# Performance work log

Measured on AMD Instinct MI355X. Metric: run time of the kernel, lower is better.

The kernel has to match this reference:

```python
import jax, jax.numpy as jnp
import numpy as np
import math

B, T, P, E, H = 4, 64, 256, 512, 8
D = E // H
LN_EPS = 1e-5


def setup_inputs() -> dict:
    key = jax.random.key(0)
    ks = jax.random.split(key, 6)
    s = 0.02  # weight init scale
    return {
        "x": jax.random.normal(ks[0], (B, T, P, E), jnp.float32),
        "Wq": jax.random.normal(ks[1], (E, E), jnp.float32) * s,
        "bq": jnp.zeros((E,), jnp.float32),
        "Wk": jax.random.normal(ks[2], (E, E), jnp.float32) * s,
        "bk": jnp.zeros((E,), jnp.float32),
        "Wv": jax.random.normal(ks[3], (E, E), jnp.float32) * s,
        "bv": jnp.zeros((E,), jnp.float32),
        "Wo": jax.random.normal(ks[4], (E, E), jnp.float32) * s,
        "bo": jnp.zeros((E,), jnp.float32),
        "ln_g": jnp.ones((E,), jnp.float32),
        "ln_b": jnp.zeros((E,), jnp.float32),
    }


def _proj(x, W, b):
    # torch nn.Linear: y = x @ W.T + b
    return jnp.einsum('btpe,fe->btpf', x, W) + b


def _heads(y):
    # b t p (h d) -> b p h t d
    b, t, p, e = y.shape
    return y.reshape(b, t, p, H, D).transpose(0, 2, 3, 1, 4)


def reference(x, Wq, bq, Wk, bk, Wv, bv, Wo, bo, ln_g, ln_b):
    b, t, p, e = x.shape
    q = _heads(_proj(x, Wq, bq))  # [B,P,H,T,D]
    k = _heads(_proj(x, Wk, bk))
    v = _heads(_proj(x, Wv, bv))

    scores = jnp.einsum('bphtd,bphsd->bphts', q, k) / math.sqrt(D)
    causal_mask = jnp.triu(jnp.ones((t, t), dtype=bool), k=1)  # True above diag
    scores = jnp.where(causal_mask, -jnp.inf, scores)
    attn = jax.nn.softmax(scores, axis=-1)
    o = jnp.einsum('bphts,bphsd->bphtd', attn, v)

    # b p h t d -> b t p (h d)
    o = o.transpose(0, 3, 1, 2, 4).reshape(b, t, p, e)
    attn_out = jnp.einsum('btpe,fe->btpf', o, Wo) + bo

    y = x + attn_out
    # AdaptiveNormalizer with conditioning=None -> plain LayerNorm over E
    mu = jnp.mean(y, axis=-1, keepdims=True)
    var = jnp.var(y, axis=-1, keepdims=True)
    return (y - mu) * jax.lax.rsqrt(var + LN_EPS) * ln_g + ln_b
```

## Files before the change

### kernel.cpp

```cpp
#include <hip/hip_runtime.h>
#include <stdint.h>

#define B_ 4
#define T_ 64
#define P_ 256
#define E_ 512
#define H_ 8
#define D_ 64
#define NF 1536
#define MCH 16384

typedef unsigned short u16;
typedef __attribute__((ext_vector_type(8))) __bf16 bf16x8;
typedef __attribute__((ext_vector_type(4))) float f32x4;

__device__ __forceinline__ u16 f2bf(float x) {
  union { float f; uint32_t u; } a; a.f = x;
  uint32_t u = a.u;
  uint32_t r = (u + 0x7FFFu + ((u >> 16) & 1u)) >> 16;
  return (u16)r;
}

__device__ __forceinline__ bf16x8 ld8(const u16* p) {
  union { uint4 u; bf16x8 b; } t;
  t.u = *reinterpret_cast<const uint4*>(p);
  return t.b;
}

typedef __attribute__((address_space(3))) void lds_void;
typedef __attribute__((address_space(1))) void g_void;
__device__ __forceinline__ void gl_lds16(const void* g, void* l) {
  __builtin_amdgcn_global_load_lds((g_void*)g, (lds_void*)l, 16, 0, 0);
}

__device__ __forceinline__ f32x4 mfma16(bf16x8 a, bf16x8 b, f32x4 c) {
  return __builtin_amdgcn_mfma_f32_16x16x32_bf16(a, b, c, 0, 0, 0);
}

#define SBAR() __builtin_amdgcn_s_barrier()

__global__ void cvt_bf16(const float* __restrict__ src, u16* __restrict__ dst, int n8) {
  int i = blockIdx.x * blockDim.x + threadIdx.x;
  if (i >= n8) return;
  const float4* s = reinterpret_cast<const float4*>(src) + (size_t)i * 2;
  float4 a = s[0], b = s[1];
  union { u16 u[8]; uint4 v; } t;
  t.u[0] = f2bf(a.x); t.u[1] = f2bf(a.y); t.u[2] = f2bf(a.z); t.u[3] = f2bf(a.w);
  t.u[4] = f2bf(b.x); t.u[5] = f2bf(b.y); t.u[6] = f2bf(b.z); t.u[7] = f2bf(b.w);
  reinterpret_cast<uint4*>(dst)[i] = t.v;
}

__global__ void cvt_w(const float* __restrict__ Wq, const float* __restrict__ Wk,
                      const float* __restrict__ Wv, const float* __restrict__ Wo,
                      u16* __restrict__ wqkv, u16* __restrict__ wobf) {
  int idx = blockIdx.x * blockDim.x + threadIdx.x;
  int w = idx >> 15;
  int off = idx & 32767;
  const float* s = (w == 0) ? Wq : (w == 1) ? Wk : (w == 2) ? Wv : Wo;
  const float4* sp = reinterpret_cast<const float4*>(s) + (size_t)off * 2;
  float4 a = sp[0], b = sp[1];
  union { u16 u[8]; uint4 v; } t;
  t.u[0] = f2bf(a.x); t.u[1] = f2bf(a.y); t.u[2] = f2bf(a.z); t.u[3] = f2bf(a.w);
  t.u[4] = f2bf(b.x); t.u[5] = f2bf(b.y); t.u[6] = f2bf(b.z); t.u[7] = f2bf(b.w);
  if (w < 3) reinterpret_cast<uint4*>(wqkv)[w * 32768 + off] = t.v;
  else       reinterpret_cast<uint4*>(wobf)[off] = t.v;
}

#define K1_MFMA(MB)                                                         \
  __builtin_amdgcn_s_setprio(1);                                            \
  _Pragma("unroll") for (int i = 0; i < 4; i++)                             \
  _Pragma("unroll") for (int j = 0; j < 4; j++)                             \
    acc[(MB) + i][j] = mfma16(af[i], bfv[j], acc[(MB) + i][j]);             \
  __builtin_amdgcn_s_setprio(0);

#define K1_READA(E, HH, MB)                                                 \
  _Pragma("unroll") for (int i = 0; i < 4; i++)                             \
    af[i] = ld8(ldsA + ((E) * 2 + (HH)) * 8192 +                            \
                (wr * 128 + ((MB) + i) * 16 + l15) * 32 + xr8);

#define K1_READB(E, HH)                                                     \
  _Pragma("unroll") for (int j = 0; j < 4; j++)                             \
    bfv[j] = ld8(ldsB + ((E) * 2 + (HH)) * 8192 +                           \
                 (wc * 64 + j * 16 + l15) * 32 + xr8);

__global__ __launch_bounds__(512, 2) void k1_qkv(
    const u16* __restrict__ xbf,
    const u16* __restrict__ wqkv,
    const float* __restrict__ bq, const float* __restrict__ bk, const float* __restrict__ bv,
    u16* __restrict__ qkv)
{
  __shared__ u16 lds[65536];
  u16* ldsA = lds;
  u16* ldsB = lds + 32768;

  const int tid = threadIdx.x;
  const int lane = tid & 63, wid = tid >> 6;
  const int wr = wid >> 2, wc = wid & 3;
  const int g4 = lane >> 4, l15 = lane & 15;
  const int xr8 = (g4 ^ ((l15 >> 1) & 3)) * 8;

  const int cpx = gridDim.x >> 3;
  const int logical = (blockIdx.x & 7) * cpx + (blockIdx.x >> 3);
  const int m0 = (logical / 6) * 256;
  const int n0 = (logical % 6) * 256;

  const u16* ga = xbf + (size_t)m0 * E_;
  const u16* gb = wqkv + (size_t)n0 * E_;

  const int r0 = tid >> 2;
  const int c0 = ((tid & 3) ^ ((tid >> 3) & 3)) * 8;

  auto stageA = [&](int e, int h, int kt) {
    const int kc = kt * 64 + h * 32;
    u16* base = ldsA + (e * 2 + h) * 8192;
    gl_lds16(ga + (size_t)r0 * E_ + kc + c0, base + wid * 512);
    gl_lds16(ga + (size_t)(r0 + 128) * E_ + kc + c0, base + 4096 + wid * 512);
  };
  auto stageB = [&](int e, int h, int kt) {
    const int kc = kt * 64 + h * 32;
    u16* base = ldsB + (e * 2 + h) * 8192;
    gl_lds16(gb + (size_t)r0 * E_ + kc + c0, base + wid * 512);
    gl_lds16(gb + (size_t)(r0 + 128) * E_ + kc + c0, base + 4096 + wid * 512);
  };

  f32x4 acc[8][4];
#pragma unroll
  for (int i = 0; i < 8; i++)
#pragma unroll
    for (int j = 0; j < 4; j++) { f32x4 z = {0.f, 0.f, 0.f, 0.f}; acc[i][j] = z; }

  stageA(0, 0, 0); stageB(0, 0, 0);
  stageA(0, 1, 0); stageB(0, 1, 0);
  stageA(1, 0, 1); stageB(1, 0, 1);
  asm volatile("s_waitcnt vmcnt(8)" ::: "memory");
  SBAR();

#pragma unroll 2
  for (int s = 0; s < 8; ++s) {
    const int e = s & 1;
    bf16x8 af[4], bfv[4];
    K1_READA(e, 0, 0)
    K1_READB(e, 0)
    if (s < 7) stageA(e ^ 1, 1, s + 1);
    SBAR();
    K1_MFMA(0)
    SBAR();
    K1_READA(e, 0, 4)
    if (s < 7) stageB(e ^ 1, 1, s + 1);
    if (s < 7) { asm volatile("s_waitcnt vmcnt(8)" ::: "memory"); }
    else       { asm volatile("s_waitcnt vmcnt(0)" ::: "memory"); }
    SBAR();
    K1_MFMA(4)
    SBAR();
    K1_READA(e, 1, 0)
    K1_READB(e, 1)
    if (s < 6) stageA(e, 0, s + 2);
    SBAR();
    K1_MFMA(0)
    SBAR();
    K1_READA(e, 1, 4)
    if (s < 6) stageB(e, 0, s + 2);
    if (s < 6)      { asm volatile("s_waitcnt vmcnt(8)" ::: "memory"); }
    else if (s == 6){ asm volatile("s_waitcnt vmcnt(4)" ::: "memory"); }
    SBAR();
    K1_MFMA(4)
    SBAR();
  }

  float bias4[4];
#pragma unroll
  for (int ni = 0; ni < 4; ni++) {
    const int fcol = n0 + wc * 64 + ni * 16 + l15;
    bias4[ni] = fcol < 512 ? bq[fcol] : (fcol < 1024 ? bk[fcol - 512] : bv[fcol - 1024]);
  }
  const int fbase = n0 + wc * 64 + l15;
#pragma unroll
  for (int mi = 0; mi < 8; mi++)
#pragma unroll
    for (int r = 0; r < 4; r++) {
      const size_t row = m0 + wr * 128 + mi * 16 + g4 * 4 + r;
      u16* dst = qkv + row * NF + fbase;
#pragma unroll
      for (int ni = 0; ni < 4; ni++)
        dst[ni * 16] = f2bf(acc[mi][ni][r] + bias4[ni]);
    }
}

__global__ __launch_bounds__(256) void k2_attn(
    const u16* __restrict__ qkv,
    u16* __restrict__ o)
{
  __shared__ u16 Pl[4][64 * 72];
  const int tid = threadIdx.x, lane = tid & 63, wid = tid >> 6;
  const int gw = blockIdx.x * 4 + wid;
  const int b = gw >> 11;
  const int g = gw & 2047;
  const int h = g & 7, p = g >> 3;
  const int g4 = lane >> 4;
  const size_t ts = (size_t)P_ * NF;
  const u16* qb = qkv + (size_t)b * MCH * NF + (size_t)p * NF + h * D_;
  const u16* kb = qb + 512;
  const u16* vb = qb + 1024;
  u16* ob = o + (size_t)b * MCH * E_;

  bf16x8 qf[4][2], kf[4][2];
#pragma unroll
  for (int i = 0; i < 4; i++)
#pragma unroll
    for (int ks = 0; ks < 2; ks++) {
      const int rr = i * 16 + (lane & 15);
      const int dc = ks * 32 + g4 * 8;
      qf[i][ks] = ld8(qb + (size_t)rr * ts + dc);
      kf[i][ks] = ld8(kb + (size_t)rr * ts + dc);
    }
  f32x4 S[4][4];
#pragma unroll
  for (int i = 0; i < 4; i++)
#pragma unroll
    for (int j = 0; j < 4; j++) { f32x4 z = {0.f, 0.f, 0.f, 0.f}; S[i][j] = z; }
#pragma unroll
  for (int ks = 0; ks < 2; ks++)
#pragma unroll
    for (int mi = 0; mi < 4; mi++)
#pragma unroll
      for (int ni = 0; ni < 4; ni++)
        S[mi][ni] = mfma16(qf[mi][ks], kf[ni][ks], S[mi][ni]);

  u16* pw = &Pl[wid][0];
#pragma unroll
  for (int mi = 0; mi < 4; mi++)
#pragma unroll
    for (int r = 0; r < 4; r++) {
      const int t = mi * 16 + g4 * 4 + r;
      float v[4]; float mx = -1e30f;
#pragma unroll
      for (int ni = 0; ni < 4; ni++) {
        const int s = ni * 16 + (lane & 15);
        v[ni] = (s <= t) ? S[mi][ni][r] * 0.125f : -1e30f;
        mx = fmaxf(mx, v[ni]);
      }
      mx = fmaxf(mx, __shfl_xor(mx, 1));
      mx = fmaxf(mx, __shfl_xor(mx, 2));
      mx = fmaxf(mx, __shfl_xor(mx, 4));
      mx = fmaxf(mx, __shfl_xor(mx, 8));
      float sum = 0.f; float pv[4];
#pragma unroll
      for (int ni = 0; ni < 4; ni++) {
        const int s = ni * 16 + (lane & 15);
        pv[ni] = (s <= t) ? __expf(v[ni] - mx) : 0.f;
        sum += pv[ni];
      }
      sum += __shfl_xor(sum, 1);
      sum += __shfl_xor(sum, 2);
      sum += __shfl_xor(sum, 4);
      sum += __shfl_xor(sum, 8);
      const float inv = 1.0f / sum;
#pragma unroll
      for (int ni = 0; ni < 4; ni++) {
        const int s = ni * 16 + (lane & 15);
        pw[t * 72 + s] = f2bf(pv[ni] * inv);
      }
    }
  __syncthreads();

  f32x4 O[4][4];
#pragma unroll
  for (int i = 0; i < 4; i++)
#pragma unroll
    for (int j = 0; j < 4; j++) { f32x4 z = {0.f, 0.f, 0.f, 0.f}; O[i][j] = z; }
#pragma unroll
  for (int ks = 0; ks < 2; ks++) {
    bf16x8 pa[4], vf[4];
#pragma unroll
    for (int mi = 0; mi < 4; mi++)
      pa[mi] = ld8(pw + (mi * 16 + (lane & 15)) * 72 + ks * 32 + g4 * 8);
#pragma unroll
    for (int ni = 0; ni < 4; ni++) {
      union { u16 u[8]; bf16x8 b; } tv;
#pragma unroll
      for (int j = 0; j < 8; j++) {
        const int s = ks * 32 + g4 * 8 + j;
        tv.u[j] = vb[(size_t)s * ts + ni * 16 + (lane & 15)];
      }
      vf[ni] = tv.b;
    }
#pragma unroll
    for (int mi = 0; mi < 4; mi++)
#pragma unroll
      for (int ni = 0; ni < 4; ni++)
        O[mi][ni] = mfma16(pa[mi], vf[ni], O[mi][ni]);
  }
#pragma unroll
  for (int mi = 0; mi < 4; mi++)
#pragma unroll
    for (int ni = 0; ni < 4; ni++)
#pragma unroll
      for (int r = 0; r < 4; r++) {
        const int t = mi * 16 + g4 * 4 + r;
        const int d = ni * 16 + (lane & 15);
        ob[((size_t)t * P_ + p) * E_ + h * D_ + d] = f2bf(O[mi][ni][r]);
      }
}

__global__ __launch_bounds__(512) void k3_out(
    const u16* __restrict__ obf,
    const u16* __restrict__ wo,
    const float* __restrict__ bo,
    const float* __restrict__ x,
    const float* __restrict__ lng, const float* __restrict__ lnb,
    float* __restrict__ out)
{
  __shared__ u16 As[2][128 * 32];
  __shared__ u16 Bs[2][512 * 32];
  __shared__ float redS[128][8];
  __shared__ float redQ[128][8];
  const int tid = threadIdx.x, lane = tid & 63, wid = tid >> 6;
  const int m0 = blockIdx.x * 128;
  const int g4 = lane >> 4, l15 = lane & 15;
  const int lr = lane >> 2;
  const int lc = (lane & 3) * 8;

  f32x4 acc[8][4];
#pragma unroll
  for (int i = 0; i < 8; i++)
#pragma unroll
    for (int j = 0; j < 4; j++) { f32x4 z = {0.f, 0.f, 0.f, 0.f}; acc[i][j] = z; }

  const u16* ga = obf + (size_t)m0 * E_;

  auto stage = [&](int buf, int kt) {
    const int k0 = kt * 32;
    gl_lds16(ga + (size_t)(wid * 16 + lr) * E_ + k0 + lc, &As[buf][wid * 512]);
#pragma unroll
    for (int p = 0; p < 4; ++p) {
      const int ch = wid * 4 + p;
      gl_lds16(wo + (size_t)(ch * 16 + lr) * E_ + k0 + lc, &Bs[buf][ch * 512]);
    }
  };

  stage(0, 0);
  __syncthreads();
  int cur = 0;
  for (int kt = 0; kt < 16; ++kt) {
    if (kt < 15) stage(cur ^ 1, kt + 1);
    const int fc = g4 * 8;
    bf16x8 af[8], bfr[4];
#pragma unroll
    for (int mi = 0; mi < 8; mi++) af[mi] = ld8(&As[cur][(mi * 16 + l15) * 32 + fc]);
#pragma unroll
    for (int ni = 0; ni < 4; ni++) bfr[ni] = ld8(&Bs[cur][(wid * 64 + ni * 16 + l15) * 32 + fc]);
#pragma unroll
    for (int mi = 0; mi < 8; mi++)
#pragma unroll
      for (int ni = 0; ni < 4; ni++)
        acc[mi][ni] = mfma16(af[mi], bfr[ni], acc[mi][ni]);
    __syncthreads();
    cur ^= 1;
  }

  float gg[4], bb[4], bof[4];
#pragma unroll
  for (int ni = 0; ni < 4; ni++) {
    const int f = wid * 64 + ni * 16 + l15;
    gg[ni] = lng[f]; bb[ni] = lnb[f]; bof[ni] = bo[f];
  }
#pragma unroll
  for (int mi = 0; mi < 8; mi++)
#pragma unroll
    for (int r = 0; r < 4; r++) {
      const int n = m0 + mi * 16 + g4 * 4 + r;
#pragma unroll
      for (int ni = 0; ni < 4; ni++) {
        const int f = wid * 64 + ni * 16 + l15;
        acc[mi][ni][r] += bof[ni] + x[(size_t)n * E_ + f];
      }
    }
#pragma unroll
  for (int mi = 0; mi < 8; mi++)
#pragma unroll
    for (int r = 0; r < 4; r++) {
      float s = 0.f, q = 0.f;
#pragma unroll
      for (int ni = 0; ni < 4; ni++) { const float y = acc[mi][ni][r]; s += y; q += y * y; }
      s += __shfl_xor(s, 1); q += __shfl_xor(q, 1);
      s += __shfl_xor(s, 2); q += __shfl_xor(q, 2);
      s += __shfl_xor(s, 4); q += __shfl_xor(q, 4);
      s += __shfl_xor(s, 8); q += __shfl_xor(q, 8);
      if (l15 == 0) {
        const int rl = mi * 16 + g4 * 4 + r;
        redS[rl][wid] = s; redQ[rl][wid] = q;
      }
    }
  __syncthreads();
#pragma unroll
  for (int mi = 0; mi < 8; mi++)
#pragma unroll
    for (int r = 0; r < 4; r++) {
      const int rl = mi * 16 + g4 * 4 + r;
      float Sx = 0.f, Qx = 0.f;
#pragma unroll
      for (int w = 0; w < 8; w++) { Sx += redS[rl][w]; Qx += redQ[rl][w]; }
      const float mean = Sx * (1.0f / 512.0f);
      const float var = Qx * (1.0f / 512.0f) - mean * mean;
      const float rs = rsqrtf(var + 1e-5f);
      const int n = m0 + rl;
#pragma unroll
      for (int ni = 0; ni < 4; ni++) {
        const int f = wid * 64 + ni * 16 + l15;
        out[(size_t)n * E_ + f] = (acc[mi][ni][r] - mean) * rs * gg[ni] + bb[ni];
      }
    }
}

extern "C" void kernel_launch(void* const* d_in, const int* in_sizes, int n_in,
                              void* d_out, int out_size, void* d_ws, size_t ws_size,
                              hipStream_t stream) {
  const float* x   = (const float*)d_in[0];
  const float* Wq  = (const float*)d_in[1];
  const float* bq  = (const float*)d_in[2];
  const float* Wk  = (const float*)d_in[3];
  const float* bk  = (const float*)d_in[4];
  const float* Wv  = (const float*)d_in[5];
  const float* bv  = (const float*)d_in[6];
  const float* Wo  = (const float*)d_in[7];
  const float* bo  = (const float*)d_in[8];
  const float* lng = (const float*)d_in[9];
  const float* lnb = (const float*)d_in[10];
  float* out = (float*)d_out;
  uint8_t* ws = (uint8_t*)d_ws;

  const size_t NEED_BIG = 270532608ULL;
  if (ws_size >= NEED_BIG) {
    u16* wqkv = (u16*)(ws);
    u16* wobf = (u16*)(ws + 1572864);
    u16* xbf  = (u16*)(ws + 2097152);
    u16* qkvc = (u16*)(ws + 69206016);
    u16* obf  = xbf;

    cvt_w<<<512, 256, 0, stream>>>(Wq, Wk, Wv, Wo, wqkv, wobf);
    cvt_bf16<<<16384, 256, 0, stream>>>(x, xbf, B_ * MCH * E_ / 8);
    k1_qkv<<<1536, 512, 0, stream>>>(xbf, wqkv, bq, bk, bv, qkvc);
    k2_attn<<<2048, 256, 0, stream>>>(qkvc, obf);
    k3_out<<<512, 512, 0, stream>>>(obf, wobf, bo, x, lng, lnb, out);
  } else {
    u16* xbf  = (u16*)(ws);
    u16* qkvc = (u16*)(ws + 16777216);
    u16* obf  = (u16*)(ws + 67108864);
    u16* wqkv = (u16*)(ws + 83886080);
    u16* wobf = (u16*)(ws + 85458944);

    cvt_w<<<512, 256, 0, stream>>>(Wq, Wk, Wv, Wo, wqkv, wobf);
    for (int b = 0; b < B_; ++b) {
      const float* xb = x + (size_t)b * MCH * E_;
      cvt_bf16<<<4096, 256, 0, stream>>>(xb, xbf, MCH * E_ / 8);
      k1_qkv<<<384, 512, 0, stream>>>(xbf, wqkv, bq, bk, bv, qkvc);
      k2_attn<<<512, 256, 0, stream>>>(qkvc, obf);
      k3_out<<<128, 512, 0, stream>>>(obf, wobf, bo, xb, lng, lnb, out + (size_t)b * MCH * E_);
    }
  }
}
```

Measured before the change: 402.1 us.

## Restructure output-projection GEMM: 64-row tiles, direct A loads, swizzled LDS for Wo

The output projection plus LayerNorm kernel now processes 64 rows per block instead of 128, doubling the grid. The A operand (attention output) is read straight from global memory into registers instead of being staged through LDS. The Wo tile staging uses an XOR swizzle to avoid LDS bank conflicts and explicit vmcnt waits with raw barriers. MFMA priority boosting and a launch-bounds occupancy hint are added. Smaller tiles mean Wo is reused across fewer rows per block, and the direct global loads of A may be less coalesced, in exchange for higher occupancy and fewer LDS conflicts.

```diff
diff --git a/kernel.cpp b/kernel.cpp
--- a/kernel.cpp
+++ b/kernel.cpp
@@ -302,7 +302,7 @@
       }
 }
 
-__global__ __launch_bounds__(512) void k3_out(
+__global__ __launch_bounds__(512, 4) void k3_out(
     const u16* __restrict__ obf,
     const u16* __restrict__ wo,
     const float* __restrict__ bo,
@@ -310,73 +310,83 @@
     const float* __restrict__ lng, const float* __restrict__ lnb,
     float* __restrict__ out)
 {
-  __shared__ u16 As[2][128 * 32];
   __shared__ u16 Bs[2][512 * 32];
-  __shared__ float redS[128][8];
-  __shared__ float redQ[128][8];
+  __shared__ float redS[64][8];
+  __shared__ float redQ[64][8];
   const int tid = threadIdx.x, lane = tid & 63, wid = tid >> 6;
-  const int m0 = blockIdx.x * 128;
   const int g4 = lane >> 4, l15 = lane & 15;
-  const int lr = lane >> 2;
-  const int lc = (lane & 3) * 8;
-
-  f32x4 acc[8][4];
-#pragma unroll
-  for (int i = 0; i < 8; i++)
+  const int xr8 = (g4 ^ ((l15 >> 1) & 3)) * 8;
+  const int m0 = blockIdx.x * 64;
+
+  const int srow = lane >> 2;
+  const int scol = ((lane & 3) ^ ((srow >> 1) & 3)) * 8;
+
+  const u16* ga = obf + (size_t)m0 * E_;
+
+  auto stageB = [&](int e, int kt) {
+    const int k0 = kt * 32;
+#pragma unroll
+    for (int p = 0; p < 4; ++p) {
+      const int gz = wid * 4 + p;
+      gl_lds16(wo + (size_t)(gz * 16 + srow) * E_ + k0 + scol, &Bs[e][gz * 512]);
+    }
+  };
+
+  f32x4 acc[4][4];
+#pragma unroll
+  for (int i = 0; i < 4; i++)
 #pragma unroll
     for (int j = 0; j < 4; j++) { f32x4 z = {0.f, 0.f, 0.f, 0.f}; acc[i][j] = z; }
 
-  const u16* ga = obf + (size_t)m0 * E_;
-
-  auto stage = [&](int buf, int kt) {
-    const int k0 = kt * 32;
-    gl_lds16(ga + (size_t)(wid * 16 + lr) * E_ + k0 + lc, &As[buf][wid * 512]);
-#pragma unroll
-    for (int p = 0; p < 4; ++p) {
-      const int ch = wid * 4 + p;
-      gl_lds16(wo + (size_t)(ch * 16 + lr) * E_ + k0 + lc, &Bs[buf][ch * 512]);
-    }
-  };
-
-  stage(0, 0);
-  __syncthreads();
-  int cur = 0;
+  stageB(0, 0);
+  asm volatile("s_waitcnt vmcnt(0)" ::: "memory");
+  SBAR();
+
+#pragma unroll 2
   for (int kt = 0; kt < 16; ++kt) {
-    if (kt < 15) stage(cur ^ 1, kt + 1);
-    const int fc = g4 * 8;
-    bf16x8 af[8], bfr[4];
-#pragma unroll
-    for (int mi = 0; mi < 8; mi++) af[mi] = ld8(&As[cur][(mi * 16 + l15) * 32 + fc]);
-#pragma unroll
-    for (int ni = 0; ni < 4; ni++) bfr[ni] = ld8(&Bs[cur][(wid * 64 + ni * 16 + l15) * 32 + fc]);
-#pragma unroll
-    for (int mi = 0; mi < 8; mi++)
-#pragma unroll
-      for (int ni = 0; ni < 4; ni++)
-        acc[mi][ni] = mfma16(af[mi], bfr[ni], acc[mi][ni]);
-    __syncthreads();
-    cur ^= 1;
-  }
-
+    const int e = kt & 1;
+    bf16x8 af[4], bfv[4];
+#pragma unroll
+    for (int mi = 0; mi < 4; mi++)
+      af[mi] = ld8(ga + (size_t)(mi * 16 + l15) * E_ + kt * 32 + g4 * 8);
+    if (kt < 15) {
+      stageB(e ^ 1, kt + 1);
+      asm volatile("s_waitcnt vmcnt(4)" ::: "memory");
+    } else {
+      asm volatile("s_waitcnt vmcnt(0)" ::: "memory");
+    }
+    SBAR();
+#pragma unroll
+    for (int ni = 0; ni < 4; ni++)
+      bfv[ni] = ld8(&Bs[e][(wid * 64 + ni * 16 + l15) * 32 + xr8]);
+    __builtin_amdgcn_s_setprio(1);
+#pragma unroll
+    for (int mi = 0; mi < 4; mi++)
+#pragma unroll
+      for (int ni = 0; ni < 4; ni++)
+        acc[mi][ni] = mfma16(af[mi], bfv[ni], acc[mi][ni]);
+    __builtin_amdgcn_s_setprio(0);
+    SBAR();
+  }
+
+  const int fb = wid * 64 + l15;
   float gg[4], bb[4], bof[4];
 #pragma unroll
   for (int ni = 0; ni < 4; ni++) {
-    const int f = wid * 64 + ni * 16 + l15;
+    const int f = fb + ni * 16;
     gg[ni] = lng[f]; bb[ni] = lnb[f]; bof[ni] = bo[f];
   }
 #pragma unroll
-  for (int mi = 0; mi < 8; mi++)
+  for (int mi = 0; mi < 4; mi++)
 #pragma unroll
     for (int r = 0; r < 4; r++) {
       const int n = m0 + mi * 16 + g4 * 4 + r;
 #pragma unroll
-      for (int ni = 0; ni < 4; ni++) {
-        const int f = wid * 64 + ni * 16 + l15;
-        acc[mi][ni][r] += bof[ni] + x[(size_t)n * E_ + f];
-      }
-    }
-#pragma unroll
-  for (int mi = 0; mi < 8; mi++)
+      for (int ni = 0; ni < 4; ni++)
+        acc[mi][ni][r] += bof[ni] + x[(size_t)n * E_ + fb + ni * 16];
+    }
+#pragma unroll
+  for (int mi = 0; mi < 4; mi++)
 #pragma unroll
     for (int r = 0; r < 4; r++) {
       float s = 0.f, q = 0.f;
@@ -393,7 +403,7 @@
     }
   __syncthreads();
 #pragma unroll
-  for (int mi = 0; mi < 8; mi++)
+  for (int mi = 0; mi < 4; mi++)
 #pragma unroll
     for (int r = 0; r < 4; r++) {
       const int rl = mi * 16 + g4 * 4 + r;
@@ -405,10 +415,8 @@
       const float rs = rsqrtf(var + 1e-5f);
       const int n = m0 + rl;
 #pragma unroll
-      for (int ni = 0; ni < 4; ni++) {
-        const int f = wid * 64 + ni * 16 + l15;
-        out[(size_t)n * E_ + f] = (acc[mi][ni][r] - mean) * rs * gg[ni] + bb[ni];
-      }
+      for (int ni = 0; ni < 4; ni++)
+        out[(size_t)n * E_ + fb + ni * 16] = (acc[mi][ni][r] - mean) * rs * gg[ni] + bb[ni];
     }
 }
 
@@ -441,7 +449,7 @@
     cvt_bf16<<<16384, 256, 0, stream>>>(x, xbf, B_ * MCH * E_ / 8);
     k1_qkv<<<1536, 512, 0, stream>>>(xbf, wqkv, bq, bk, bv, qkvc);
     k2_attn<<<2048, 256, 0, stream>>>(qkvc, obf);
-    k3_out<<<512, 512, 0, stream>>>(obf, wobf, bo, x, lng, lnb, out);
+    k3_out<<<1024, 512, 0, stream>>>(obf, wobf, bo, x, lng, lnb, out);
   } else {
     u16* xbf  = (u16*)(ws);
     u16* qkvc = (u16*)(ws + 16777216);
@@ -455,7 +463,7 @@
       cvt_bf16<<<4096, 256, 0, stream>>>(xb, xbf, MCH * E_ / 8);
       k1_qkv<<<384, 512, 0, stream>>>(xbf, wqkv, bq, bk, bv, qkvc);
       k2_attn<<<512, 256, 0, stream>>>(qkvc, obf);
-      k3_out<<<128, 512, 0, stream>>>(obf, wobf, bo, xb, lng, lnb, out + (size_t)b * MCH * E_);
-    }
-  }
-}
+      k3_out<<<256, 512, 0, stream>>>(obf, wobf, bo, xb, lng, lnb, out + (size_t)b * MCH * E_);
+    }
+  }
+}
```

After: 443.0 us. 10.2% more time.

## Deepen k3_out LDS pipeline with swizzled layout and fine-grained waitcnt scheduling

Applied to the files above, without the earlier changes.

Rewrites the output-projection GEMM main loop to stage K=64 per iteration in two half-tiles across a deeper multi-buffer LDS ring (160KB shared). It uses explicit vmcnt waits instead of full syncs, and an XOR swizzle on LDS columns to cut bank conflicts. MFMA bursts are wrapped in s_setprio to favour the matrix work. The goal is to hide global-to-LDS load latency and cut per-iteration barrier stalls. The trade-off is a large LDS footprint that limits occupancy, and hand-counted waitcnt values that are fragile.

```diff
diff --git a/kernel.cpp b/kernel.cpp
--- a/kernel.cpp
+++ b/kernel.cpp
@@ -302,7 +302,7 @@
       }
 }
 
-__global__ __launch_bounds__(512) void k3_out(
+__global__ __launch_bounds__(512, 2) void k3_out(
     const u16* __restrict__ obf,
     const u16* __restrict__ wo,
     const float* __restrict__ bo,
@@ -310,15 +310,44 @@
     const float* __restrict__ lng, const float* __restrict__ lnb,
     float* __restrict__ out)
 {
-  __shared__ u16 As[2][128 * 32];
-  __shared__ u16 Bs[2][512 * 32];
-  __shared__ float redS[128][8];
-  __shared__ float redQ[128][8];
+  __shared__ u16 S[81920];
+  u16* SA = S;
+  u16* SB = S + 16384;
+  float* redS = (float*)S;
+  float* redQ = (float*)S + 1024;
+
   const int tid = threadIdx.x, lane = tid & 63, wid = tid >> 6;
+  const int g4 = lane >> 4, l15 = lane & 15;
+  const int xr8 = (g4 ^ ((l15 >> 1) & 3)) * 8;
   const int m0 = blockIdx.x * 128;
-  const int g4 = lane >> 4, l15 = lane & 15;
-  const int lr = lane >> 2;
-  const int lc = (lane & 3) * 8;
+
+  const u16* ga = obf + (size_t)m0 * E_;
+  const int r0 = tid >> 2;
+  const int c0 = ((tid & 3) ^ ((tid >> 3) & 3)) * 8;
+
+  auto stage = [&](int e, int h, int kt) {
+    const int kc = kt * 64 + h * 32;
+    gl_lds16(ga + (size_t)r0 * E_ + kc + c0, SA + (e * 2 + h) * 4096 + wid * 512);
+    u16* bb = SB + (e * 2 + h) * 16384;
+#pragma unroll
+    for (int p = 0; p < 4; ++p) {
+      const int row = p * 128 + r0;
+      gl_lds16(wo + (size_t)row * E_ + kc + c0, bb + p * 4096 + wid * 512);
+    }
+  };
+
+#define K3_READA(E, HH)                                                     \
+  _Pragma("unroll") for (int i = 0; i < 8; i++)                             \
+    af[i] = ld8(SA + ((E) * 2 + (HH)) * 4096 + (i * 16 + l15) * 32 + xr8);
+#define K3_READB(E, HH)                                                     \
+  _Pragma("unroll") for (int j = 0; j < 4; j++)                             \
+    bfv[j] = ld8(SB + ((E) * 2 + (HH)) * 16384 + (wid * 64 + j * 16 + l15) * 32 + xr8);
+#define K3_MFMA()                                                           \
+  __builtin_amdgcn_s_setprio(1);                                            \
+  _Pragma("unroll") for (int i = 0; i < 8; i++)                             \
+  _Pragma("unroll") for (int j = 0; j < 4; j++)                             \
+    acc[i][j] = mfma16(af[i], bfv[j], acc[i][j]);                           \
+  __builtin_amdgcn_s_setprio(0);
 
   f32x4 acc[8][4];
 #pragma unroll
@@ -326,43 +355,40 @@
 #pragma unroll
     for (int j = 0; j < 4; j++) { f32x4 z = {0.f, 0.f, 0.f, 0.f}; acc[i][j] = z; }
 
-  const u16* ga = obf + (size_t)m0 * E_;
-
-  auto stage = [&](int buf, int kt) {
-    const int k0 = kt * 32;
-    gl_lds16(ga + (size_t)(wid * 16 + lr) * E_ + k0 + lc, &As[buf][wid * 512]);
-#pragma unroll
-    for (int p = 0; p < 4; ++p) {
-      const int ch = wid * 4 + p;
-      gl_lds16(wo + (size_t)(ch * 16 + lr) * E_ + k0 + lc, &Bs[buf][ch * 512]);
-    }
-  };
-
-  stage(0, 0);
-  __syncthreads();
-  int cur = 0;
-  for (int kt = 0; kt < 16; ++kt) {
-    if (kt < 15) stage(cur ^ 1, kt + 1);
-    const int fc = g4 * 8;
-    bf16x8 af[8], bfr[4];
-#pragma unroll
-    for (int mi = 0; mi < 8; mi++) af[mi] = ld8(&As[cur][(mi * 16 + l15) * 32 + fc]);
-#pragma unroll
-    for (int ni = 0; ni < 4; ni++) bfr[ni] = ld8(&Bs[cur][(wid * 64 + ni * 16 + l15) * 32 + fc]);
-#pragma unroll
-    for (int mi = 0; mi < 8; mi++)
-#pragma unroll
-      for (int ni = 0; ni < 4; ni++)
-        acc[mi][ni] = mfma16(af[mi], bfr[ni], acc[mi][ni]);
-    __syncthreads();
-    cur ^= 1;
-  }
-
-  float gg[4], bb[4], bof[4];
+  stage(0, 0, 0);
+  stage(0, 1, 0);
+  stage(1, 0, 1);
+  asm volatile("s_waitcnt vmcnt(10)" ::: "memory");
+  SBAR();
+
+#pragma unroll
+  for (int t = 0; t < 8; ++t) {
+    const int e = t & 1;
+    bf16x8 af[8], bfv[4];
+    K3_READA(e, 0)
+    K3_READB(e, 0)
+    if (t < 7) stage(e ^ 1, 1, t + 1);
+    if (t < 7) { asm volatile("s_waitcnt vmcnt(10)" ::: "memory"); }
+    else       { asm volatile("s_waitcnt vmcnt(0)" ::: "memory"); }
+    SBAR();
+    K3_MFMA()
+    SBAR();
+    K3_READA(e, 1)
+    K3_READB(e, 1)
+    if (t < 6) stage(e, 0, t + 2);
+    if (t < 6)      { asm volatile("s_waitcnt vmcnt(10)" ::: "memory"); }
+    else if (t == 6){ asm volatile("s_waitcnt vmcnt(5)" ::: "memory"); }
+    SBAR();
+    K3_MFMA()
+    SBAR();
+  }
+
+  const int fb = wid * 64 + l15;
+  float gg[4], bb2[4], bof[4];
 #pragma unroll
   for (int ni = 0; ni < 4; ni++) {
-    const int f = wid * 64 + ni * 16 + l15;
-    gg[ni] = lng[f]; bb[ni] = lnb[f]; bof[ni] = bo[f];
+    const int f = fb + ni * 16;
+    gg[ni] = lng[f]; bb2[ni] = lnb[f]; bof[ni] = bo[f];
   }
 #pragma unroll
   for (int mi = 0; mi < 8; mi++)
@@ -370,10 +396,8 @@
     for (int r = 0; r < 4; r++) {
       const int n = m0 + mi * 16 + g4 * 4 + r;
 #pragma unroll
-      for (int ni = 0; ni < 4; ni++) {
-        const int f = wid * 64 + ni * 16 + l15;
-        acc[mi][ni][r] += bof[ni] + x[(size_t)n * E_ + f];
-      }
+      for (int ni = 0; ni < 4; ni++)
+        acc[mi][ni][r] += bof[ni] + x[(size_t)n * E_ + fb + ni * 16];
     }
 #pragma unroll
   for (int mi = 0; mi < 8; mi++)
@@ -388,7 +412,7 @@
       s += __shfl_xor(s, 8); q += __shfl_xor(q, 8);
       if (l15 == 0) {
         const int rl = mi * 16 + g4 * 4 + r;
-        redS[rl][wid] = s; redQ[rl][wid] = q;
+        redS[rl * 8 + wid] = s; redQ[rl * 8 + wid] = q;
       }
     }
   __syncthreads();
@@ -399,16 +423,14 @@
       const int rl = mi * 16 + g4 * 4 + r;
       float Sx = 0.f, Qx = 0.f;
 #pragma unroll
-      for (int w = 0; w < 8; w++) { Sx += redS[rl][w]; Qx += redQ[rl][w]; }
+      for (int w = 0; w < 8; w++) { Sx += redS[rl * 8 + w]; Qx += redQ[rl * 8 + w]; }
       const float mean = Sx * (1.0f / 512.0f);
       const float var = Qx * (1.0f / 512.0f) - mean * mean;
       const float rs = rsqrtf(var + 1e-5f);
       const int n = m0 + rl;
 #pragma unroll
-      for (int ni = 0; ni < 4; ni++) {
-        const int f = wid * 64 + ni * 16 + l15;
-        out[(size_t)n * E_ + f] = (acc[mi][ni][r] - mean) * rs * gg[ni] + bb[ni];
-      }
+      for (int ni = 0; ni < 4; ni++)
+        out[(size_t)n * E_ + fb + ni * 16] = (acc[mi][ni][r] - mean) * rs * gg[ni] + bb2[ni];
     }
 }
 
```

Result: faster. 379.5 us (-5.6%).
